# Kernel optimization log

Measured on AMD Instinct MI355X. Metric: run time of the kernel, lower is better.

## Reference

```python
import jax, jax.numpy as jnp
import numpy as np

D_MODEL = 1024
NUM_HEADS = 16
D_K = D_MODEL // NUM_HEADS
THETA = 10000.0
SEQ_LEN = 4096


def setup_inputs() -> dict:
    key = jax.random.key(0)
    ks = jax.random.split(key, 5)
    std = (2.0 / (D_MODEL + D_MODEL)) ** 0.5
    x = jax.random.normal(ks[0], (1, SEQ_LEN, D_MODEL), dtype=jnp.float32)
    Wq = jax.random.normal(ks[1], (D_MODEL, D_MODEL), dtype=jnp.float32) * std
    Wk = jax.random.normal(ks[2], (D_MODEL, D_MODEL), dtype=jnp.float32) * std
    Wv = jax.random.normal(ks[3], (D_MODEL, D_MODEL), dtype=jnp.float32) * std
    Wo = jax.random.normal(ks[4], (D_MODEL, D_MODEL), dtype=jnp.float32) * std
    return {"x": x, "Wq": Wq, "Wk": Wk, "Wv": Wv, "Wo": Wo}


def _rope(x, cos, sin):
    # x: [B, H, S, d_k]; cos/sin: [S, d_k//2] broadcast over B,H
    x_even = x[..., ::2]
    x_odd = x[..., 1::2]
    r_even = x_even * cos - x_odd * sin
    r_odd = x_even * sin + x_odd * cos
    # re-interleave: stack on last axis then flatten pairs
    return jnp.stack([r_even, r_odd], axis=-1).reshape(x.shape)


def _forward(x, Wq, Wk, Wv, Wo):
    B, S, _ = x.shape
    # projections (weight stored [out, in])
    q = jnp.einsum('bsd,od->bso', x, Wq)
    k = jnp.einsum('bsd,od->bso', x, Wk)
    v = jnp.einsum('bsd,od->bso', x, Wv)
    # split heads -> [B, H, S, d_k]
    q = q.reshape(B, S, NUM_HEADS, D_K).transpose(0, 2, 1, 3)
    k = k.reshape(B, S, NUM_HEADS, D_K).transpose(0, 2, 1, 3)
    v = v.reshape(B, S, NUM_HEADS, D_K).transpose(0, 2, 1, 3)
    # RoPE tables
    freqs_d = 1.0 / (THETA ** (jnp.arange(0, D_K, 2, dtype=jnp.float32) / D_K))
    pos = jnp.arange(S, dtype=jnp.float32)
    freqs = pos[:, None] * freqs_d[None, :]  # [S, d_k//2]
    cos, sin = jnp.cos(freqs), jnp.sin(freqs)
    q = _rope(q, cos, sin)
    k = _rope(k, cos, sin)
    # scaled dot-product attention with causal mask
    scores = jnp.einsum('bhqd,bhkd->bhqk', q, k) / (D_K ** 0.5)
    causal = jnp.tril(jnp.ones((S, S), dtype=bool))
    scores = jnp.where(causal, scores, -jnp.inf)
    weights = jax.nn.softmax(scores, axis=-1)
    out = jnp.einsum('bhqk,bhkd->bhqd', weights, v)
    out = out.transpose(0, 2, 1, 3).reshape(B, S, D_MODEL)
    return jnp.einsum('bsd,od->bso', out, Wo)


def reference(x, Wq, Wk, Wv, Wo):
    return _forward(x, Wq, Wk, Wv, Wo)
```

## Files before the change

### kernel.cpp

```cpp
#include <hip/hip_runtime.h>
#include <math.h>

#define SEQ 4096
#define DMODEL 1024
#define NHEAD 16
#define DKH 64

typedef __attribute__((ext_vector_type(8))) short bf16x8;
typedef __attribute__((ext_vector_type(4))) float f32x4;

__device__ __forceinline__ ushort f2b(float x) {
    unsigned u = __float_as_uint(x);
    return (ushort)((u + 0x7fffu + ((u >> 16) & 1u)) >> 16);
}
__device__ __forceinline__ float b2f(ushort u) {
    return __uint_as_float(((unsigned)u) << 16);
}

#define DPP_ROR_F(x, ctrl) \
    __int_as_float(__builtin_amdgcn_update_dpp(__float_as_int(x), __float_as_int(x), (ctrl), 0xf, 0xf, false))

__device__ __forceinline__ float rowmax16(float x) {
    x = fmaxf(x, DPP_ROR_F(x, 0x121));
    x = fmaxf(x, DPP_ROR_F(x, 0x122));
    x = fmaxf(x, DPP_ROR_F(x, 0x124));
    x = fmaxf(x, DPP_ROR_F(x, 0x128));
    return x;
}
__device__ __forceinline__ float rowsum16(float x) {
    x += DPP_ROR_F(x, 0x121);
    x += DPP_ROR_F(x, 0x122);
    x += DPP_ROR_F(x, 0x124);
    x += DPP_ROR_F(x, 0x128);
    return x;
}

__global__ __launch_bounds__(256)
void conv_bf16(const float* __restrict__ x,  const float* __restrict__ wq,
               const float* __restrict__ wk, const float* __restrict__ wv,
               const float* __restrict__ wo,
               ushort* __restrict__ xb,  ushort* __restrict__ wqb,
               ushort* __restrict__ wkb, ushort* __restrict__ wvb,
               ushort* __restrict__ wob) {
    const int b = blockIdx.x;
    const float* src; ushort* dst; int idx;
    if (b < 4096) {
        src = x; dst = xb; idx = b * 256 + threadIdx.x;
    } else {
        int t = b - 4096;
        int which = t >> 10;
        idx = (t & 1023) * 256 + threadIdx.x;
        if      (which == 0) { src = wq; dst = wqb; }
        else if (which == 1) { src = wk; dst = wkb; }
        else if (which == 2) { src = wv; dst = wvb; }
        else                 { src = wo; dst = wob; }
    }
    float4 f = ((const float4*)src)[idx];
    ushort4 o;
    o.x = f2b(f.x); o.y = f2b(f.y); o.z = f2b(f.z); o.w = f2b(f.w);
    ((ushort4*)dst)[idx] = o;
}

#define GSTR 40

template<bool OUT_BF16>
__global__ __launch_bounds__(256)
void gemm_bf16(const ushort* __restrict__ A, const ushort* __restrict__ B,
               void* __restrict__ Cv, int M, int N, int K) {
    __shared__ __attribute__((aligned(16))) ushort As[128 * GSTR];
    __shared__ __attribute__((aligned(16))) ushort Bs[128 * GSTR];

    const int tid  = threadIdx.x;
    const int lane = tid & 63;
    const int w    = tid >> 6;
    const int wr   = w >> 1, wc = w & 1;
    const int lrow = lane & 15, lgrp = lane >> 4;
    const int m0 = blockIdx.y * 128;
    const int n0 = blockIdx.x * 128;

    const int srow = tid >> 2;
    const int skc  = (tid & 3) * 8;
    const ushort* Ap0 = A + (size_t)(m0 + srow) * K + skc;
    const ushort* Ap1 = Ap0 + (size_t)64 * K;
    const ushort* Bp0 = B + (size_t)(n0 + srow) * K + skc;
    const ushort* Bp1 = Bp0 + (size_t)64 * K;
    ushort* sA0 = &As[srow * GSTR + skc];
    ushort* sA1 = &As[(srow + 64) * GSTR + skc];
    ushort* sB0 = &Bs[srow * GSTR + skc];
    ushort* sB1 = &Bs[(srow + 64) * GSTR + skc];

    f32x4 acc[4][4];
#pragma unroll
    for (int i = 0; i < 4; i++)
#pragma unroll
        for (int j = 0; j < 4; j++) acc[i][j] = (f32x4){0.f, 0.f, 0.f, 0.f};

    bf16x8 ra0 = *(const bf16x8*)(Ap0);
    bf16x8 ra1 = *(const bf16x8*)(Ap1);
    bf16x8 rb0 = *(const bf16x8*)(Bp0);
    bf16x8 rb1 = *(const bf16x8*)(Bp1);

    const int NT = K >> 5;
    for (int kt = 0; kt < NT; kt++) {
        __syncthreads();
        *(bf16x8*)sA0 = ra0;  *(bf16x8*)sA1 = ra1;
        *(bf16x8*)sB0 = rb0;  *(bf16x8*)sB1 = rb1;
        __syncthreads();

        if (kt + 1 < NT) {
            const int ko = (kt + 1) * 32;
            ra0 = *(const bf16x8*)(Ap0 + ko);
            ra1 = *(const bf16x8*)(Ap1 + ko);
            rb0 = *(const bf16x8*)(Bp0 + ko);
            rb1 = *(const bf16x8*)(Bp1 + ko);
        }

        bf16x8 af[4], bfr[4];
#pragma unroll
        for (int i = 0; i < 4; i++)
            af[i] = *(const bf16x8*)&As[(wr * 64 + i * 16 + lrow) * GSTR + lgrp * 8];
#pragma unroll
        for (int j = 0; j < 4; j++)
            bfr[j] = *(const bf16x8*)&Bs[(wc * 64 + j * 16 + lrow) * GSTR + lgrp * 8];
#pragma unroll
        for (int i = 0; i < 4; i++)
#pragma unroll
            for (int j = 0; j < 4; j++)
                acc[i][j] = __builtin_amdgcn_mfma_f32_16x16x32_bf16(af[i], bfr[j], acc[i][j], 0, 0, 0);
    }

#pragma unroll
    for (int i = 0; i < 4; i++) {
#pragma unroll
        for (int j = 0; j < 4; j++) {
#pragma unroll
            for (int r = 0; r < 4; r++) {
                const size_t row = m0 + wr * 64 + i * 16 + lgrp * 4 + r;
                const size_t col = n0 + wc * 64 + j * 16 + lrow;
                if constexpr (OUT_BF16)
                    ((ushort*)Cv)[row * N + col] = f2b(acc[i][j][r]);
                else
                    ((float*)Cv)[row * N + col] = acc[i][j][r];
            }
        }
    }
}

__global__ __launch_bounds__(256)
void rope_bf16(ushort* __restrict__ q, ushort* __restrict__ k) {
    int idx = blockIdx.x * 256 + threadIdx.x;
    if (idx >= SEQ * (DMODEL / 2)) return;
    int s  = idx >> 9;
    int j  = idx & 511;
    int hh = j >> 5;
    int i  = j & 31;
    const float LOG1E4_OVER32 = 0.28782313662425572f;
    float freq = __expf(-(float)i * LOG1E4_OVER32);
    float ang  = (float)s * freq;
    float c, sn;
    __sincosf(ang, &sn, &c);
    size_t base = (size_t)s * DMODEL + hh * DKH + 2 * i;
    float e = b2f(q[base]), o_ = b2f(q[base + 1]);
    q[base]     = f2b(e * c - o_ * sn);
    q[base + 1] = f2b(e * sn + o_ * c);
    e = b2f(k[base]); o_ = b2f(k[base + 1]);
    k[base]     = f2b(e * c - o_ * sn);
    k[base + 1] = f2b(e * sn + o_ * c);
}

#define LSTR 72

__global__ __launch_bounds__(256)
void attn_mfma(const ushort* __restrict__ Q, const ushort* __restrict__ K,
               const ushort* __restrict__ V, ushort* __restrict__ O) {
    __shared__ __attribute__((aligned(16))) ushort Ks[64 * LSTR];
    __shared__ __attribute__((aligned(16))) ushort Vs[64 * LSTR];
    __shared__ __attribute__((aligned(16))) ushort Ps[4][16 * LSTR];

    const int tid  = threadIdx.x;
    const int w    = tid >> 6;
    const int lane = tid & 63;
    const int lrow = lane & 15;
    const int lgrp = lane >> 4;
    const int h    = blockIdx.y;
    const int qi   = (int)gridDim.x - 1 - (int)blockIdx.x;
    const int qbase = qi * 64;

    const int qr = qbase + w * 16 + lrow;
    const ushort* qp = Q + (size_t)qr * DMODEL + h * DKH + lgrp * 8;
    bf16x8 qfrag[2];
    qfrag[0] = *(const bf16x8*)(qp);
    qfrag[1] = *(const bf16x8*)(qp + 32);

    f32x4 o_acc[4];
#pragma unroll
    for (int t = 0; t < 4; t++) o_acc[t] = (f32x4){0.f, 0.f, 0.f, 0.f};
    float m_r[4], l_r[4];
#pragma unroll
    for (int r = 0; r < 4; r++) { m_r[r] = -INFINITY; l_r[r] = 0.f; }

    const int row0 = tid >> 3;
    const int col0 = (tid & 7) * 8;
    const ushort* Kp = K + (size_t)h * DKH;
    const ushort* Vp = V + (size_t)h * DKH;

    const int ktmax = qi;
    bf16x8 rk[2], rv[2];
#pragma unroll
    for (int cc = 0; cc < 2; cc++) {
        const int row = row0 + cc * 32;
        rk[cc] = *(const bf16x8*)(Kp + (size_t)row * DMODEL + col0);
        rv[cc] = *(const bf16x8*)(Vp + (size_t)row * DMODEL + col0);
    }

    for (int kt = 0; kt <= ktmax; kt++) {
        const int kbase = kt * 64;
        __syncthreads();
#pragma unroll
        for (int cc = 0; cc < 2; cc++) {
            const int row = row0 + cc * 32;
            *(bf16x8*)&Ks[row * LSTR + col0] = rk[cc];
            const int vrow = row ^ (col0 & 56);
#pragma unroll
            for (int jj = 0; jj < 8; jj++)
                Vs[(col0 + jj) * LSTR + vrow] = (ushort)rv[cc][jj];
        }
        __syncthreads();

        if (kt < ktmax) {
            const size_t nb = (size_t)(kbase + 64) * DMODEL;
#pragma unroll
            for (int cc = 0; cc < 2; cc++) {
                const int row = row0 + cc * 32;
                rk[cc] = *(const bf16x8*)(Kp + nb + (size_t)row * DMODEL + col0);
                rv[cc] = *(const bf16x8*)(Vp + nb + (size_t)row * DMODEL + col0);
            }
        }

        f32x4 s[4];
#pragma unroll
        for (int n = 0; n < 4; n++) {
            f32x4 acc = (f32x4){0.f, 0.f, 0.f, 0.f};
#pragma unroll
            for (int ks = 0; ks < 2; ks++) {
                bf16x8 kf = *(const bf16x8*)&Ks[(n * 16 + lrow) * LSTR + lgrp * 8 + ks * 32];
                acc = __builtin_amdgcn_mfma_f32_16x16x32_bf16(qfrag[ks], kf, acc, 0, 0, 0);
            }
            s[n] = acc;
        }

        const int myq = qbase + w * 16 + lgrp * 4;
#pragma unroll
        for (int n = 0; n < 4; n++) {
            const int key = kbase + n * 16 + lrow;
#pragma unroll
            for (int r = 0; r < 4; r++)
                s[n][r] = (key > myq + r) ? -INFINITY : s[n][r] * 0.125f;
        }

        float alpha[4];
#pragma unroll
        for (int r = 0; r < 4; r++) {
            float t0 = fmaxf(fmaxf(s[0][r], s[1][r]), fmaxf(s[2][r], s[3][r]));
            float mnew = fmaxf(m_r[r], rowmax16(t0));
            alpha[r] = __expf(m_r[r] - mnew);
            m_r[r] = mnew;
        }
#pragma unroll
        for (int t = 0; t < 4; t++)
#pragma unroll
            for (int r = 0; r < 4; r++) o_acc[t][r] *= alpha[r];

        float psum[4] = {0.f, 0.f, 0.f, 0.f};
#pragma unroll
        for (int n = 0; n < 4; n++) {
#pragma unroll
            for (int r = 0; r < 4; r++) {
                float p = __expf(s[n][r] - m_r[r]);
                psum[r] += p;
                Ps[w][(lgrp * 4 + r) * LSTR + n * 16 + lrow] = f2b(p);
            }
        }
#pragma unroll
        for (int r = 0; r < 4; r++)
            l_r[r] = l_r[r] * alpha[r] + rowsum16(psum[r]);

#pragma unroll
        for (int ks = 0; ks < 2; ks++) {
            bf16x8 pa = *(const bf16x8*)&Ps[w][lrow * LSTR + lgrp * 8 + ks * 32];
#pragma unroll
            for (int t = 0; t < 4; t++) {
                const int xr = (2 * t + (lrow >> 3)) << 3;
                bf16x8 vb = *(const bf16x8*)&Vs[(t * 16 + lrow) * LSTR + ((lgrp * 8 + ks * 32) ^ xr)];
                o_acc[t] = __builtin_amdgcn_mfma_f32_16x16x32_bf16(pa, vb, o_acc[t], 0, 0, 0);
            }
        }
    }

    float invl[4];
#pragma unroll
    for (int r = 0; r < 4; r++) invl[r] = 1.0f / l_r[r];
    ushort* op = O + (size_t)(qbase + w * 16) * DMODEL + h * DKH;
#pragma unroll
    for (int t = 0; t < 4; t++)
#pragma unroll
        for (int r = 0; r < 4; r++)
            op[(size_t)(lgrp * 4 + r) * DMODEL + t * 16 + lrow] = f2b(o_acc[t][r] * invl[r]);
}

extern "C" void kernel_launch(void* const* d_in, const int* in_sizes, int n_in,
                              void* d_out, int out_size, void* d_ws, size_t ws_size,
                              hipStream_t stream) {
    const float* x  = (const float*)d_in[0];
    const float* Wq = (const float*)d_in[1];
    const float* Wk = (const float*)d_in[2];
    const float* Wv = (const float*)d_in[3];
    const float* Wo = (const float*)d_in[4];
    float* out = (float*)d_out;

    const size_t NM = (size_t)SEQ * DMODEL;
    const size_t NW = (size_t)DMODEL * DMODEL;
    ushort* qb  = (ushort*)d_ws;
    ushort* kb  = qb + NM;
    ushort* vb  = kb + NM;
    ushort* ob  = vb + NM;
    ushort* xb  = ob + NM;
    ushort* wqb = xb + NM;
    ushort* wkb = wqb + NW;
    ushort* wvb = wkb + NW;
    ushort* wob = wvb + NW;

    conv_bf16<<<8192, 256, 0, stream>>>(x, Wq, Wk, Wv, Wo, xb, wqb, wkb, wvb, wob);

    dim3 ggrid(DMODEL / 128, SEQ / 128);
    gemm_bf16<true><<<ggrid, 256, 0, stream>>>(xb, wqb, qb, SEQ, DMODEL, DMODEL);
    gemm_bf16<true><<<ggrid, 256, 0, stream>>>(xb, wkb, kb, SEQ, DMODEL, DMODEL);
    gemm_bf16<true><<<ggrid, 256, 0, stream>>>(xb, wvb, vb, SEQ, DMODEL, DMODEL);

    rope_bf16<<<SEQ * (DMODEL / 2) / 256, 256, 0, stream>>>(qb, kb);

    attn_mfma<<<dim3(SEQ / 64, NHEAD), 256, 0, stream>>>(qb, kb, vb, ob);

    gemm_bf16<false><<<ggrid, 256, 0, stream>>>(ob, wob, out, SEQ, DMODEL, DMODEL);
}
```

Before: 367.4 us.

## Fuse QKV projections into one GEMM and streamline attention softmax

The three Q/K/V projection GEMMs become a single launch over a 3072-wide N dimension, which relies on wqb/wkb/wvb being contiguous and routes outputs to the qb/kb/vb buffers by column block. In attention, the causal mask is applied only on the diagonal tile, softmax moves to exp2 with a pre-scaled log2e factor, and rescaling of the output accumulator is skipped when no row max grows (wave-level any). The row sum is computed by an MFMA against a ones vector instead of DPP reductions, and s_setprio raises wave priority around the MFMA sections. These changes cut launch overhead, per-tile VALU work and transcendental cost, at the price of some extra MFMA work for the row sum.

```diff
diff --git a/kernel.cpp b/kernel.cpp
--- a/kernel.cpp
+++ b/kernel.cpp
@@ -25,13 +25,6 @@
     x = fmaxf(x, DPP_ROR_F(x, 0x122));
     x = fmaxf(x, DPP_ROR_F(x, 0x124));
     x = fmaxf(x, DPP_ROR_F(x, 0x128));
-    return x;
-}
-__device__ __forceinline__ float rowsum16(float x) {
-    x += DPP_ROR_F(x, 0x121);
-    x += DPP_ROR_F(x, 0x122);
-    x += DPP_ROR_F(x, 0x124);
-    x += DPP_ROR_F(x, 0x128);
     return x;
 }
 
@@ -63,7 +56,7 @@
 
 #define GSTR 40
 
-template<bool OUT_BF16>
+template<int MODE>
 __global__ __launch_bounds__(256)
 void gemm_bf16(const ushort* __restrict__ A, const ushort* __restrict__ B,
                void* __restrict__ Cv, int M, int N, int K) {
@@ -136,11 +129,17 @@
 #pragma unroll
             for (int r = 0; r < 4; r++) {
                 const size_t row = m0 + wr * 64 + i * 16 + lgrp * 4 + r;
-                const size_t col = n0 + wc * 64 + j * 16 + lrow;
-                if constexpr (OUT_BF16)
-                    ((ushort*)Cv)[row * N + col] = f2b(acc[i][j][r]);
-                else
-                    ((float*)Cv)[row * N + col] = acc[i][j][r];
+                if constexpr (MODE == 2) {
+                    ushort* dst = (ushort*)Cv + (size_t)(n0 >> 10) * ((size_t)SEQ * DMODEL);
+                    const size_t col = (n0 & 1023) + wc * 64 + j * 16 + lrow;
+                    dst[row * DMODEL + col] = f2b(acc[i][j][r]);
+                } else {
+                    const size_t col = n0 + wc * 64 + j * 16 + lrow;
+                    if constexpr (MODE == 1)
+                        ((ushort*)Cv)[row * N + col] = f2b(acc[i][j][r]);
+                    else
+                        ((float*)Cv)[row * N + col] = acc[i][j][r];
+                }
             }
         }
     }
@@ -169,6 +168,7 @@
 }
 
 #define LSTR 72
+#define SCALE2 0.18033688011112042f
 
 __global__ __launch_bounds__(256)
 void attn_mfma(const ushort* __restrict__ Q, const ushort* __restrict__ K,
@@ -192,12 +192,17 @@
     qfrag[0] = *(const bf16x8*)(qp);
     qfrag[1] = *(const bf16x8*)(qp + 32);
 
+    bf16x8 ones;
+#pragma unroll
+    for (int j = 0; j < 8; j++) ones[j] = (short)0x3F80;
+
     f32x4 o_acc[4];
 #pragma unroll
     for (int t = 0; t < 4; t++) o_acc[t] = (f32x4){0.f, 0.f, 0.f, 0.f};
-    float m_r[4], l_r[4];
-#pragma unroll
-    for (int r = 0; r < 4; r++) { m_r[r] = -INFINITY; l_r[r] = 0.f; }
+    f32x4 acc_l = (f32x4){0.f, 0.f, 0.f, 0.f};
+    float m_r[4];
+#pragma unroll
+    for (int r = 0; r < 4; r++) m_r[r] = -INFINITY;
 
     const int row0 = tid >> 3;
     const int col0 = (tid & 7) * 8;
@@ -238,6 +243,7 @@
         }
 
         f32x4 s[4];
+        __builtin_amdgcn_s_setprio(1);
 #pragma unroll
         for (int n = 0; n < 4; n++) {
             f32x4 acc = (f32x4){0.f, 0.f, 0.f, 0.f};
@@ -248,46 +254,59 @@
             }
             s[n] = acc;
         }
-
-        const int myq = qbase + w * 16 + lgrp * 4;
-#pragma unroll
-        for (int n = 0; n < 4; n++) {
-            const int key = kbase + n * 16 + lrow;
-#pragma unroll
-            for (int r = 0; r < 4; r++)
-                s[n][r] = (key > myq + r) ? -INFINITY : s[n][r] * 0.125f;
-        }
-
-        float alpha[4];
+        __builtin_amdgcn_s_setprio(0);
+
+        if (kt == ktmax) {
+            const int myq = qbase + w * 16 + lgrp * 4;
+#pragma unroll
+            for (int n = 0; n < 4; n++) {
+                const int key = kbase + n * 16 + lrow;
+#pragma unroll
+                for (int r = 0; r < 4; r++)
+                    s[n][r] = (key > myq + r) ? -INFINITY : s[n][r] * SCALE2;
+            }
+        } else {
+#pragma unroll
+            for (int n = 0; n < 4; n++)
+#pragma unroll
+                for (int r = 0; r < 4; r++) s[n][r] *= SCALE2;
+        }
+
+        float rmax[4];
 #pragma unroll
         for (int r = 0; r < 4; r++) {
             float t0 = fmaxf(fmaxf(s[0][r], s[1][r]), fmaxf(s[2][r], s[3][r]));
-            float mnew = fmaxf(m_r[r], rowmax16(t0));
-            alpha[r] = __expf(m_r[r] - mnew);
-            m_r[r] = mnew;
-        }
-#pragma unroll
-        for (int t = 0; t < 4; t++)
-#pragma unroll
-            for (int r = 0; r < 4; r++) o_acc[t][r] *= alpha[r];
-
-        float psum[4] = {0.f, 0.f, 0.f, 0.f};
+            rmax[r] = rowmax16(t0);
+        }
+        bool grew = false;
+#pragma unroll
+        for (int r = 0; r < 4; r++) grew = grew || (rmax[r] > m_r[r]);
+        if (__any((int)grew)) {
+#pragma unroll
+            for (int r = 0; r < 4; r++) {
+                float mnew = fmaxf(m_r[r], rmax[r]);
+                float al = exp2f(m_r[r] - mnew);
+                m_r[r] = mnew;
+                acc_l[r] *= al;
+#pragma unroll
+                for (int t = 0; t < 4; t++) o_acc[t][r] *= al;
+            }
+        }
+
 #pragma unroll
         for (int n = 0; n < 4; n++) {
 #pragma unroll
             for (int r = 0; r < 4; r++) {
-                float p = __expf(s[n][r] - m_r[r]);
-                psum[r] += p;
+                float p = exp2f(s[n][r] - m_r[r]);
                 Ps[w][(lgrp * 4 + r) * LSTR + n * 16 + lrow] = f2b(p);
             }
         }
-#pragma unroll
-        for (int r = 0; r < 4; r++)
-            l_r[r] = l_r[r] * alpha[r] + rowsum16(psum[r]);
-
+
+        __builtin_amdgcn_s_setprio(1);
 #pragma unroll
         for (int ks = 0; ks < 2; ks++) {
             bf16x8 pa = *(const bf16x8*)&Ps[w][lrow * LSTR + lgrp * 8 + ks * 32];
+            acc_l = __builtin_amdgcn_mfma_f32_16x16x32_bf16(pa, ones, acc_l, 0, 0, 0);
 #pragma unroll
             for (int t = 0; t < 4; t++) {
                 const int xr = (2 * t + (lrow >> 3)) << 3;
@@ -295,11 +314,12 @@
                 o_acc[t] = __builtin_amdgcn_mfma_f32_16x16x32_bf16(pa, vb, o_acc[t], 0, 0, 0);
             }
         }
+        __builtin_amdgcn_s_setprio(0);
     }
 
     float invl[4];
 #pragma unroll
-    for (int r = 0; r < 4; r++) invl[r] = 1.0f / l_r[r];
+    for (int r = 0; r < 4; r++) invl[r] = 1.0f / acc_l[r];
     ushort* op = O + (size_t)(qbase + w * 16) * DMODEL + h * DKH;
 #pragma unroll
     for (int t = 0; t < 4; t++)
@@ -332,14 +352,13 @@
 
     conv_bf16<<<8192, 256, 0, stream>>>(x, Wq, Wk, Wv, Wo, xb, wqb, wkb, wvb, wob);
 
-    dim3 ggrid(DMODEL / 128, SEQ / 128);
-    gemm_bf16<true><<<ggrid, 256, 0, stream>>>(xb, wqb, qb, SEQ, DMODEL, DMODEL);
-    gemm_bf16<true><<<ggrid, 256, 0, stream>>>(xb, wkb, kb, SEQ, DMODEL, DMODEL);
-    gemm_bf16<true><<<ggrid, 256, 0, stream>>>(xb, wvb, vb, SEQ, DMODEL, DMODEL);
+    gemm_bf16<2><<<dim3(3 * DMODEL / 128, SEQ / 128), 256, 0, stream>>>(
+        xb, wqb, qb, SEQ, 3 * DMODEL, DMODEL);
 
     rope_bf16<<<SEQ * (DMODEL / 2) / 256, 256, 0, stream>>>(qb, kb);
 
     attn_mfma<<<dim3(SEQ / 64, NHEAD), 256, 0, stream>>>(qb, kb, vb, ob);
 
-    gemm_bf16<false><<<ggrid, 256, 0, stream>>>(ob, wob, out, SEQ, DMODEL, DMODEL);
-}
+    gemm_bf16<0><<<dim3(DMODEL / 128, SEQ / 128), 256, 0, stream>>>(
+        ob, wob, out, SEQ, DMODEL, DMODEL);
+}
```

After: 328.2 us. 10.7% less time.
